# Performance work log

Hardware: AMD Instinct MI355X
Metric: run time of the kernel (lower is better)

Reference implementation:

```python
import jax, jax.numpy as jnp
import numpy as np

B, T, C, H = 4, 2048, 1024, 16
D = C // H  # head_dim = 64
ROPE_BASE = 10000.0


def _rope_cos_sin(T, D, dtype):
    # inv_freq: (D/2,), freqs: (T, D/2) -> cos/sin tiled to (T, D)
    inv_freq = 1.0 / (ROPE_BASE ** (jnp.arange(0, D, 2, dtype=jnp.float32) / D))
    freqs = jnp.arange(T, dtype=jnp.float32)[:, None] * inv_freq[None, :]
    emb = jnp.concatenate([freqs, freqs], axis=-1)  # (T, D)
    return jnp.cos(emb).astype(dtype), jnp.sin(emb).astype(dtype)


def _rotate_half(x):
    x1, x2 = jnp.split(x, 2, axis=-1)
    return jnp.concatenate([-x2, x1], axis=-1)


def setup_inputs() -> dict:
    key = jax.random.key(0)
    k1, k2, k3 = jax.random.split(key, 3)
    x = jax.random.normal(k1, (B, T, C), dtype=jnp.float32)
    W_qkv = jax.random.normal(k2, (C, 3 * C), dtype=jnp.float32) * (C ** -0.5)
    b_qkv = jnp.zeros((3 * C,), dtype=jnp.float32)
    W_out = jax.random.normal(k3, (C, C), dtype=jnp.float32) * (C ** -0.5)
    b_out = jnp.zeros((C,), dtype=jnp.float32)
    return {"x": x, "W_qkv": W_qkv, "b_qkv": b_qkv, "W_out": W_out, "b_out": b_out}


def reference(x, W_qkv, b_qkv, W_out, b_out):
    Bx, Tx, Cx = x.shape
    qkv = x @ W_qkv + b_qkv                                   # (B, T, 3C)
    qkv = qkv.reshape(Bx, Tx, 3, H, D).transpose(2, 0, 3, 1, 4)  # (3, B, H, T, D)
    q, k, v = qkv[0], qkv[1], qkv[2]

    cos, sin = _rope_cos_sin(Tx, D, x.dtype)                  # (T, D) each
    q = q * cos + _rotate_half(q) * sin
    k = k * cos + _rotate_half(k) * sin

    # NOTE: original code has no 1/sqrt(D) scaling — faithful reproduction.
    att = jnp.einsum('bhtd,bhsd->bhts', q, k)                 # (B, H, T, T)
    causal = jnp.tril(jnp.ones((Tx, Tx), dtype=bool))
    att = jnp.where(causal[None, None, :, :], att, -jnp.inf)
    att = jax.nn.softmax(att, axis=-1)
    y = jnp.einsum('bhts,bhsd->bhtd', att, v)                 # (B, H, T, D)
    y = y.transpose(0, 2, 1, 3).reshape(Bx, Tx, Cx)
    return y @ W_out + b_out
```

## Files before the change

### kernel.cpp

```cpp
#include <hip/hip_runtime.h>
#include <math.h>

#define NB    4
#define T_SEQ 2048
#define CDIM  1024
#define NH    16
#define DH    64
#define NQKV  3072

typedef short bf16x8 __attribute__((ext_vector_type(8)));
typedef float f32x4  __attribute__((ext_vector_type(4)));

#define GLOBAL_AS __attribute__((address_space(1)))
#define LDS_AS    __attribute__((address_space(3)))

__device__ __forceinline__ void async16(const void* g, void* l) {
  __builtin_amdgcn_global_load_lds((const GLOBAL_AS void*)g, (LDS_AS void*)l, 16, 0, 0);
}

__device__ __forceinline__ unsigned short f2bf(float f) {
  unsigned u = __float_as_uint(f);
  unsigned r = u + 0x7FFF + ((u >> 16) & 1);
  return (unsigned short)(r >> 16);
}

#define SWZ8(row, c) ((((row) << 3) | ((c) ^ ((row) & 7))) << 3)

#define BARRIER()  asm volatile("s_barrier" ::: "memory")
#define VMCNT(n)   asm volatile("s_waitcnt vmcnt(" #n ")" ::: "memory")

__global__ __launch_bounds__(256) void rope_table(float2* __restrict__ tab) {
  int i = blockIdx.x * 256 + threadIdx.x;
  int t = i >> 5, d = i & 31;
  float inv = expf((float)d * -0.28782313662425572f);
  float s, c;
  sincosf((float)t * inv, &s, &c);
  tab[i] = make_float2(c, s);
}

__global__ __launch_bounds__(256) void convert_bf16(
    const float* __restrict__ in, unsigned short* __restrict__ out, int n4) {
  int i = blockIdx.x * 256 + threadIdx.x;
  if (i >= n4) return;
  float4 v = ((const float4*)in)[i];
  ushort4 o;
  o.x = f2bf(v.x); o.y = f2bf(v.y); o.z = f2bf(v.z); o.w = f2bf(v.w);
  ((ushort4*)out)[i] = o;
}

__global__ __launch_bounds__(256) void transpose_to_bf16(
    const float* __restrict__ in, unsigned short* __restrict__ out, int K, int N) {
  __shared__ float tile[32][33];
  int n0 = blockIdx.x << 5, k0 = blockIdx.y << 5;
  int r  = threadIdx.x >> 3;
  int c4 = (threadIdx.x & 7) << 2;
  float4 v = *(const float4*)&in[(size_t)(k0 + r) * N + n0 + c4];
  tile[r][c4 + 0] = v.x; tile[r][c4 + 1] = v.y;
  tile[r][c4 + 2] = v.z; tile[r][c4 + 3] = v.w;
  __syncthreads();
  ushort4 o;
  o.x = f2bf(tile[c4 + 0][r]); o.y = f2bf(tile[c4 + 1][r]);
  o.z = f2bf(tile[c4 + 2][r]); o.w = f2bf(tile[c4 + 3][r]);
  *(ushort4*)&out[(size_t)(n0 + r) * K + k0 + c4] = o;
}

__global__ __launch_bounds__(256) void transpose_v(
    const unsigned short* __restrict__ v, unsigned short* __restrict__ vt) {
  __shared__ unsigned short tile[64][65];
  int bh = blockIdx.y;
  int t0 = blockIdx.x << 6;
  size_t ib = (size_t)bh * (T_SEQ * DH);
  int tid = threadIdx.x;
#pragma unroll
  for (int u = 0; u < 2; ++u) {
    int f = u * 256 + tid;
    int tr = f >> 3, c = f & 7;
    bf16x8 val = *(const bf16x8*)&v[ib + (size_t)(t0 + tr) * DH + c * 8];
#pragma unroll
    for (int j = 0; j < 8; ++j) tile[tr][c * 8 + j] = (unsigned short)val[j];
  }
  __syncthreads();
#pragma unroll
  for (int u = 0; u < 2; ++u) {
    int f = u * 256 + tid;
    int d = f >> 3, c = f & 7;
    bf16x8 o;
#pragma unroll
    for (int j = 0; j < 8; ++j) o[j] = (short)tile[c * 8 + j][d];
    *(bf16x8*)&vt[ib + (size_t)d * T_SEQ + t0 + c * 8] = o;
  }
}

#define STAGE(kt, b)                                                          \
  { const unsigned short* sa_ = aSrc + (kt) * 64;                             \
    const unsigned short* sb_ = bSrc + (kt) * 64;                             \
    async16(sa_,          &As[b][d0]);                                        \
    async16(sa_ + 65536,  &As[b][d0 + 4096]);                                 \
    async16(sb_,          &Bs[b][d0]);                                        \
    async16(sb_ + 65536,  &Bs[b][d0 + 4096]);                                 \
    async16(sb_ + 131072, &Bs[b][d0 + 8192]);                                 \
    async16(sb_ + 196608, &Bs[b][d0 + 12288]); }

#define GEMM_PIPE(Aptr, Btptr)                                                \
  __shared__ short As[3][128 * 64];                                           \
  __shared__ short Bs[3][256 * 64];                                           \
  int m0 = blockIdx.y << 7, n0 = blockIdx.x << 8;                             \
  int tid = threadIdx.x;                                                      \
  int wave = tid >> 6, lane = tid & 63;                                       \
  int wm = wave >> 2, wn = wave & 3;                                          \
  int col = lane & 15, quad = lane >> 4;                                      \
  int srow = tid >> 3;                                                        \
  int schunk = (tid & 7) ^ (srow & 7);                                        \
  const unsigned short* aSrc = &Aptr[(size_t)(m0 + srow) * CDIM + schunk * 8];\
  const unsigned short* bSrc = &Btptr[(size_t)(n0 + srow) * CDIM + schunk * 8];\
  int d0 = wave * 512;      \
  f32x4 acc[4][4];                                                            \
  _Pragma("unroll") for (int mt = 0; mt < 4; ++mt)                            \
  _Pragma("unroll") for (int nt = 0; nt < 4; ++nt)                            \
    acc[mt][nt] = (f32x4){0.f, 0.f, 0.f, 0.f};                                \
  STAGE(0, 0)                                                                 \
  STAGE(1, 1)                                                                 \
  _Pragma("unroll")                                                           \
  for (int t = 0; t < 16; ++t) {                                              \
    if (t < 15) { VMCNT(6); } else { VMCNT(0); }                              \
    BARRIER();                                                                \
    if (t + 2 < 16) STAGE(t + 2, (t + 2) % 3)                                 \
    const short* A_ = As[t % 3];                                              \
    const short* B_ = Bs[t % 3];                                              \
    _Pragma("unroll") for (int ks = 0; ks < 2; ++ks) {                        \
      bf16x8 af[4], bfr[4];                                                   \
      _Pragma("unroll") for (int mt = 0; mt < 4; ++mt)                        \
        af[mt] = *(const bf16x8*)&A_[SWZ8(wm * 64 + mt * 16 + col,            \
                                          ks * 4 + quad)];                    \
      _Pragma("unroll") for (int nt = 0; nt < 4; ++nt)                        \
        bfr[nt] = *(const bf16x8*)&B_[SWZ8(wn * 64 + nt * 16 + col,           \
                                           ks * 4 + quad)];                   \
      __builtin_amdgcn_s_setprio(1);                                          \
      _Pragma("unroll") for (int mt = 0; mt < 4; ++mt)                        \
        _Pragma("unroll") for (int nt = 0; nt < 4; ++nt)                      \
          acc[mt][nt] = __builtin_amdgcn_mfma_f32_16x16x32_bf16(              \
              af[mt], bfr[nt], acc[mt][nt], 0, 0, 0);                         \
      __builtin_amdgcn_s_setprio(0);                                          \
    }                                                                         \
  }

__global__ __launch_bounds__(512, 2) void gemm_qkv_mfma(
    const unsigned short* __restrict__ A, const unsigned short* __restrict__ Bt,
    const float* __restrict__ bias, const float2* __restrict__ rope,
    unsigned short* __restrict__ qb, unsigned short* __restrict__ kb,
    unsigned short* __restrict__ vb) {
  GEMM_PIPE(A, Bt)
  int nn = n0 + wn * 64;
  int which = nn >> 10;
  int h = (nn >> 6) & 15;
  unsigned short* dst = (which == 0) ? qb : ((which == 1) ? kb : vb);
  float bv[4];
#pragma unroll
  for (int nt = 0; nt < 4; ++nt) bv[nt] = bias[nn + nt * 16 + col];
  if (which < 2) {
#pragma unroll
    for (int mt = 0; mt < 4; ++mt) {
#pragma unroll
      for (int r = 0; r < 4; ++r) {
        int m = m0 + wm * 64 + mt * 16 + quad * 4 + r;
        int bidx = m >> 11, t = m & 2047;
        float x0 = acc[mt][0][r] + bv[0];
        float x1 = acc[mt][1][r] + bv[1];
        float x2 = acc[mt][2][r] + bv[2];
        float x3 = acc[mt][3][r] + bv[3];
        float2 cs0 = rope[(t << 5) + col];
        float2 cs1 = rope[(t << 5) + col + 16];
        size_t ro = (((size_t)bidx * NH + h) * T_SEQ + t) * DH;
        dst[ro + col]      = f2bf(x0 * cs0.x - x2 * cs0.y);
        dst[ro + col + 16] = f2bf(x1 * cs1.x - x3 * cs1.y);
        dst[ro + col + 32] = f2bf(x2 * cs0.x + x0 * cs0.y);
        dst[ro + col + 48] = f2bf(x3 * cs1.x + x1 * cs1.y);
      }
    }
  } else {
#pragma unroll
    for (int mt = 0; mt < 4; ++mt) {
#pragma unroll
      for (int r = 0; r < 4; ++r) {
        int m = m0 + wm * 64 + mt * 16 + quad * 4 + r;
        int bidx = m >> 11, t = m & 2047;
        size_t ro = (((size_t)bidx * NH + h) * T_SEQ + t) * DH;
        dst[ro + col]      = f2bf(acc[mt][0][r] + bv[0]);
        dst[ro + col + 16] = f2bf(acc[mt][1][r] + bv[1]);
        dst[ro + col + 32] = f2bf(acc[mt][2][r] + bv[2]);
        dst[ro + col + 48] = f2bf(acc[mt][3][r] + bv[3]);
      }
    }
  }
}

__global__ __launch_bounds__(512, 2) void gemm_out_mfma(
    const unsigned short* __restrict__ A, const unsigned short* __restrict__ Bt,
    const float* __restrict__ bias, float* __restrict__ out) {
  GEMM_PIPE(A, Bt)
#pragma unroll
  for (int nt = 0; nt < 4; ++nt) {
    int n = n0 + wn * 64 + nt * 16 + col;
    float bv = bias[n];
#pragma unroll
    for (int mt = 0; mt < 4; ++mt) {
#pragma unroll
      for (int r = 0; r < 4; ++r) {
        int m = m0 + wm * 64 + mt * 16 + quad * 4 + r;
        out[(size_t)m * CDIM + n] = acc[mt][nt][r] + bv;
      }
    }
  }
}

__global__ __launch_bounds__(256) void attn_mfma(
    const unsigned short* __restrict__ qg, const unsigned short* __restrict__ kg,
    const unsigned short* __restrict__ vtg, unsigned short* __restrict__ yb) {
  __shared__ short Qs[128 * 64];
  __shared__ short Ks[64 * 64];
  __shared__ short Vts[64 * 64];
  __shared__ short Ps[4][32][72];
  int tid = threadIdx.x;
  int wave = tid >> 6, lane = tid & 63;
  int col = lane & 15, quad = lane >> 4;
  int bh = blockIdx.x;
  int qblk = 15 - (int)blockIdx.y;
  int qb0 = qblk << 7;
  size_t base = (size_t)bh * (T_SEQ * DH);

#pragma unroll
  for (int u = 0; u < 4; ++u) {
    int ff = u * 256 + wave * 64 + lane;
    int row = ff >> 3, cl = ff & 7;
    int cg = cl ^ (row & 7);
    async16(&qg[base + (size_t)(qb0 + row) * DH + cg * 8],
            &Qs[(u * 256 + wave * 64) * 8]);
  }

  bf16x8 ones;
#pragma unroll
  for (int j = 0; j < 8; ++j) ones[j] = (short)0x3F80;

  f32x4 oc[2][4], lsum[2];
#pragma unroll
  for (int mf = 0; mf < 2; ++mf) {
    lsum[mf] = (f32x4){0.f, 0.f, 0.f, 0.f};
#pragma unroll
    for (int dt = 0; dt < 4; ++dt) oc[mf][dt] = (f32x4){0.f, 0.f, 0.f, 0.f};
  }

  int qlo = qb0 + wave * 32;
  int qhi = qlo + 31;
  int nkb = (qblk << 1) + 2;
  for (int kb = 0; kb < nkb; ++kb) {
    int s0 = kb << 6;
    __syncthreads();
#pragma unroll
    for (int u = 0; u < 2; ++u) {
      int ff = u * 256 + wave * 64 + lane;
      int row = ff >> 3, cl = ff & 7;
      int cg = cl ^ (row & 7);
      async16(&kg[base + (size_t)(s0 + row) * DH + cg * 8],
              &Ks[(u * 256 + wave * 64) * 8]);
      async16(&vtg[base + (size_t)row * T_SEQ + s0 + cg * 8],
              &Vts[(u * 256 + wave * 64) * 8]);
    }
    __syncthreads();
    if (s0 > qhi) continue;

    f32x4 sc[2][4];
#pragma unroll
    for (int mf = 0; mf < 2; ++mf)
#pragma unroll
      for (int nt = 0; nt < 4; ++nt) sc[mf][nt] = (f32x4){0.f, 0.f, 0.f, 0.f};
#pragma unroll
    for (int kc = 0; kc < 2; ++kc) {
      bf16x8 aq0 = *(const bf16x8*)&Qs[SWZ8(wave * 32 + col,      kc * 4 + quad)];
      bf16x8 aq1 = *(const bf16x8*)&Qs[SWZ8(wave * 32 + 16 + col, kc * 4 + quad)];
#pragma unroll
      for (int nt = 0; nt < 4; ++nt) {
        bf16x8 bk = *(const bf16x8*)&Ks[SWZ8(nt * 16 + col, kc * 4 + quad)];
        sc[0][nt] = __builtin_amdgcn_mfma_f32_16x16x32_bf16(aq0, bk, sc[0][nt], 0, 0, 0);
        sc[1][nt] = __builtin_amdgcn_mfma_f32_16x16x32_bf16(aq1, bk, sc[1][nt], 0, 0, 0);
      }
    }

    if (s0 + 63 > qlo) {
#pragma unroll
      for (int mf = 0; mf < 2; ++mf)
#pragma unroll
        for (int nt = 0; nt < 4; ++nt) {
          int s_glob = s0 + nt * 16 + col;
#pragma unroll
          for (int r = 0; r < 4; ++r)
            if (s_glob > qlo + mf * 16 + quad * 4 + r) sc[mf][nt][r] = -3.0e38f;
        }
    }

#pragma unroll
    for (int mf = 0; mf < 2; ++mf)
#pragma unroll
      for (int nt = 0; nt < 4; ++nt)
#pragma unroll
        for (int r = 0; r < 4; ++r)
          Ps[wave][mf * 16 + quad * 4 + r][nt * 16 + col] =
              (short)f2bf(__expf(sc[mf][nt][r]));

#pragma unroll
    for (int kc = 0; kc < 2; ++kc) {
      bf16x8 ap0 = *(const bf16x8*)&Ps[wave][col][kc * 32 + quad * 8];
      bf16x8 ap1 = *(const bf16x8*)&Ps[wave][16 + col][kc * 32 + quad * 8];
      lsum[0] = __builtin_amdgcn_mfma_f32_16x16x32_bf16(ap0, ones, lsum[0], 0, 0, 0);
      lsum[1] = __builtin_amdgcn_mfma_f32_16x16x32_bf16(ap1, ones, lsum[1], 0, 0, 0);
#pragma unroll
      for (int dt = 0; dt < 4; ++dt) {
        bf16x8 vb = *(const bf16x8*)&Vts[SWZ8(dt * 16 + col, kc * 4 + quad)];
        oc[0][dt] = __builtin_amdgcn_mfma_f32_16x16x32_bf16(ap0, vb, oc[0][dt], 0, 0, 0);
        oc[1][dt] = __builtin_amdgcn_mfma_f32_16x16x32_bf16(ap1, vb, oc[1][dt], 0, 0, 0);
      }
    }
  }

  int b = bh >> 4, h = bh & 15;
#pragma unroll
  for (int mf = 0; mf < 2; ++mf)
#pragma unroll
    for (int dt = 0; dt < 4; ++dt) {
      int d = dt * 16 + col;
#pragma unroll
      for (int r = 0; r < 4; ++r) {
        int t = qb0 + wave * 32 + mf * 16 + quad * 4 + r;
        yb[(((size_t)b * T_SEQ + t) * NH + h) * DH + d] =
            f2bf(oc[mf][dt][r] / lsum[mf][r]);
      }
    }
}

extern "C" void kernel_launch(void* const* d_in, const int* in_sizes, int n_in,
                              void* d_out, int out_size, void* d_ws, size_t ws_size,
                              hipStream_t stream) {
  const float* x     = (const float*)d_in[0];
  const float* W_qkv = (const float*)d_in[1];
  const float* b_qkv = (const float*)d_in[2];
  const float* W_out = (const float*)d_in[3];
  const float* b_out = (const float*)d_in[4];
  float* out = (float*)d_out;

  const size_t per = (size_t)NB * NH * T_SEQ * DH;
  unsigned short* xb  = (unsigned short*)d_ws;
  unsigned short* qb  = xb + per;
  unsigned short* kbf = qb + per;
  unsigned short* vbf = kbf + per;
  unsigned short* vtb = vbf + per;
  unsigned short* yb  = vtb + per;
  unsigned short* wqt = yb + per;
  unsigned short* wot = wqt + (size_t)NQKV * CDIM;
  float2* rope = (float2*)(wot + (size_t)CDIM * CDIM);

  rope_table<<<256, 256, 0, stream>>>(rope);
  convert_bf16<<<(int)(per / 4 / 256), 256, 0, stream>>>(x, xb, (int)(per / 4));
  transpose_to_bf16<<<dim3(NQKV / 32, CDIM / 32), 256, 0, stream>>>(W_qkv, wqt, CDIM, NQKV);
  transpose_to_bf16<<<dim3(CDIM / 32, CDIM / 32), 256, 0, stream>>>(W_out, wot, CDIM, CDIM);
  gemm_qkv_mfma<<<dim3(NQKV / 256, (NB * T_SEQ) / 128), 512, 0, stream>>>(
      xb, wqt, b_qkv, rope, qb, kbf, vbf);
  transpose_v<<<dim3(T_SEQ / 64, NB * NH), 256, 0, stream>>>(vbf, vtb);
  attn_mfma<<<dim3(NB * NH, T_SEQ / 128), 256, 0, stream>>>(qb, kbf, vtb, yb);
  gemm_out_mfma<<<dim3(CDIM / 256, (NB * T_SEQ) / 128), 512, 0, stream>>>(
      yb, wot, b_out, out);
}
```

Measured before the change: 261.7 us.

## Keep Q in registers and compute transposed scores for packed P stores

Q fragments now load straight from global memory into registers and stay there, which removes the Q shared-memory tile and its async load. The QK^T MFMA is transposed (K as the A operand, Q as B), so each lane holds four consecutive key scores for one query. These are packed into bf16 pairs with v_cvt_pk_bf16_f32 and written to a swizzled P buffer as 8-byte stores instead of scalar 2-byte stores. The cost is more VGPRs per thread, with some risk to occupancy.

```diff
diff --git a/kernel.cpp b/kernel.cpp
--- a/kernel.cpp
+++ b/kernel.cpp
@@ -216,10 +216,9 @@
 __global__ __launch_bounds__(256) void attn_mfma(
     const unsigned short* __restrict__ qg, const unsigned short* __restrict__ kg,
     const unsigned short* __restrict__ vtg, unsigned short* __restrict__ yb) {
-  __shared__ short Qs[128 * 64];
   __shared__ short Ks[64 * 64];
   __shared__ short Vts[64 * 64];
-  __shared__ short Ps[4][32][72];
+  __shared__ short Ps[4][32 * 64];
   int tid = threadIdx.x;
   int wave = tid >> 6, lane = tid & 63;
   int col = lane & 15, quad = lane >> 4;
@@ -228,14 +227,13 @@
   int qb0 = qblk << 7;
   size_t base = (size_t)bh * (T_SEQ * DH);
 
-#pragma unroll
-  for (int u = 0; u < 4; ++u) {
-    int ff = u * 256 + wave * 64 + lane;
-    int row = ff >> 3, cl = ff & 7;
-    int cg = cl ^ (row & 7);
-    async16(&qg[base + (size_t)(qb0 + row) * DH + cg * 8],
-            &Qs[(u * 256 + wave * 64) * 8]);
-  }
+  bf16x8 qreg[2][2];
+#pragma unroll
+  for (int nt = 0; nt < 2; ++nt)
+#pragma unroll
+    for (int kc = 0; kc < 2; ++kc)
+      qreg[nt][kc] = *(const bf16x8*)&qg[base +
+          (size_t)(qb0 + wave * 32 + nt * 16 + col) * DH + kc * 32 + quad * 8];
 
   bf16x8 ones;
 #pragma unroll
@@ -243,10 +241,10 @@
 
   f32x4 oc[2][4], lsum[2];
 #pragma unroll
-  for (int mf = 0; mf < 2; ++mf) {
-    lsum[mf] = (f32x4){0.f, 0.f, 0.f, 0.f};
-#pragma unroll
-    for (int dt = 0; dt < 4; ++dt) oc[mf][dt] = (f32x4){0.f, 0.f, 0.f, 0.f};
+  for (int mq = 0; mq < 2; ++mq) {
+    lsum[mq] = (f32x4){0.f, 0.f, 0.f, 0.f};
+#pragma unroll
+    for (int dt = 0; dt < 4; ++dt) oc[mq][dt] = (f32x4){0.f, 0.f, 0.f, 0.f};
   }
 
   int qlo = qb0 + wave * 32;
@@ -268,48 +266,59 @@
     __syncthreads();
     if (s0 > qhi) continue;
 
-    f32x4 sc[2][4];
-#pragma unroll
-    for (int mf = 0; mf < 2; ++mf)
-#pragma unroll
-      for (int nt = 0; nt < 4; ++nt) sc[mf][nt] = (f32x4){0.f, 0.f, 0.f, 0.f};
+    f32x4 sc[4][2];
+#pragma unroll
+    for (int mf = 0; mf < 4; ++mf)
+#pragma unroll
+      for (int nt = 0; nt < 2; ++nt) sc[mf][nt] = (f32x4){0.f, 0.f, 0.f, 0.f};
 #pragma unroll
     for (int kc = 0; kc < 2; ++kc) {
-      bf16x8 aq0 = *(const bf16x8*)&Qs[SWZ8(wave * 32 + col,      kc * 4 + quad)];
-      bf16x8 aq1 = *(const bf16x8*)&Qs[SWZ8(wave * 32 + 16 + col, kc * 4 + quad)];
-#pragma unroll
-      for (int nt = 0; nt < 4; ++nt) {
-        bf16x8 bk = *(const bf16x8*)&Ks[SWZ8(nt * 16 + col, kc * 4 + quad)];
-        sc[0][nt] = __builtin_amdgcn_mfma_f32_16x16x32_bf16(aq0, bk, sc[0][nt], 0, 0, 0);
-        sc[1][nt] = __builtin_amdgcn_mfma_f32_16x16x32_bf16(aq1, bk, sc[1][nt], 0, 0, 0);
+#pragma unroll
+      for (int mf = 0; mf < 4; ++mf) {
+        bf16x8 ak = *(const bf16x8*)&Ks[SWZ8(mf * 16 + col, kc * 4 + quad)];
+        sc[mf][0] = __builtin_amdgcn_mfma_f32_16x16x32_bf16(ak, qreg[0][kc], sc[mf][0], 0, 0, 0);
+        sc[mf][1] = __builtin_amdgcn_mfma_f32_16x16x32_bf16(ak, qreg[1][kc], sc[mf][1], 0, 0, 0);
       }
     }
 
     if (s0 + 63 > qlo) {
 #pragma unroll
-      for (int mf = 0; mf < 2; ++mf)
-#pragma unroll
-        for (int nt = 0; nt < 4; ++nt) {
-          int s_glob = s0 + nt * 16 + col;
+      for (int mf = 0; mf < 4; ++mf) {
+        int kbase = s0 + mf * 16 + quad * 4;
+#pragma unroll
+        for (int nt = 0; nt < 2; ++nt) {
+          int qq = qlo + nt * 16 + col;
 #pragma unroll
           for (int r = 0; r < 4; ++r)
-            if (s_glob > qlo + mf * 16 + quad * 4 + r) sc[mf][nt][r] = -3.0e38f;
+            if (kbase + r > qq) sc[mf][nt][r] = -3.0e38f;
         }
-    }
-
-#pragma unroll
-    for (int mf = 0; mf < 2; ++mf)
-#pragma unroll
-      for (int nt = 0; nt < 4; ++nt)
-#pragma unroll
-        for (int r = 0; r < 4; ++r)
-          Ps[wave][mf * 16 + quad * 4 + r][nt * 16 + col] =
-              (short)f2bf(__expf(sc[mf][nt][r]));
+      }
+    }
+
+#pragma unroll
+    for (int nt = 0; nt < 2; ++nt) {
+      int row = nt * 16 + col;
+      int rb = row << 6;
+      int sw = row & 7;
+#pragma unroll
+      for (int mf = 0; mf < 4; ++mf) {
+        float p0 = __expf(sc[mf][nt][0]);
+        float p1 = __expf(sc[mf][nt][1]);
+        float p2 = __expf(sc[mf][nt][2]);
+        float p3 = __expf(sc[mf][nt][3]);
+        unsigned w0, w1;
+        asm("v_cvt_pk_bf16_f32 %0, %1, %2" : "=v"(w0) : "v"(p0), "v"(p1));
+        asm("v_cvt_pk_bf16_f32 %0, %1, %2" : "=v"(w1) : "v"(p2), "v"(p3));
+        int chunk = (mf << 1) | (quad >> 1);
+        int off = rb + (((chunk ^ sw) << 3) | ((quad & 1) << 2));
+        *(uint2*)&Ps[wave][off] = make_uint2(w0, w1);
+      }
+    }
 
 #pragma unroll
     for (int kc = 0; kc < 2; ++kc) {
-      bf16x8 ap0 = *(const bf16x8*)&Ps[wave][col][kc * 32 + quad * 8];
-      bf16x8 ap1 = *(const bf16x8*)&Ps[wave][16 + col][kc * 32 + quad * 8];
+      bf16x8 ap0 = *(const bf16x8*)&Ps[wave][SWZ8(col,      kc * 4 + quad)];
+      bf16x8 ap1 = *(const bf16x8*)&Ps[wave][SWZ8(16 + col, kc * 4 + quad)];
       lsum[0] = __builtin_amdgcn_mfma_f32_16x16x32_bf16(ap0, ones, lsum[0], 0, 0, 0);
       lsum[1] = __builtin_amdgcn_mfma_f32_16x16x32_bf16(ap1, ones, lsum[1], 0, 0, 0);
 #pragma unroll
@@ -323,15 +332,15 @@
 
   int b = bh >> 4, h = bh & 15;
 #pragma unroll
-  for (int mf = 0; mf < 2; ++mf)
+  for (int mq = 0; mq < 2; ++mq)
 #pragma unroll
     for (int dt = 0; dt < 4; ++dt) {
       int d = dt * 16 + col;
 #pragma unroll
       for (int r = 0; r < 4; ++r) {
-        int t = qb0 + wave * 32 + mf * 16 + quad * 4 + r;
+        int t = qb0 + wave * 32 + mq * 16 + quad * 4 + r;
         yb[(((size_t)b * T_SEQ + t) * NH + h) * DH + d] =
-            f2bf(oc[mf][dt][r] / lsum[mf][r]);
+            f2bf(oc[mq][dt][r] / lsum[mq][r]);
       }
     }
 }
```

Result: no change. 259.1 us (-1.0%).
